# Performance work log

Measured on AMD Instinct MI355X. Metric: run time of the kernel, lower is better.

Reference implementation:

```python
import jax, jax.numpy as jnp
import numpy as np

B, C, H, W = 2, 64, 128, 128
HEADS, DH = 8, 32
DN = ('NCHW', 'OIHW', 'NCHW')


def _conv(x, w, pad):
    return jax.lax.conv_general_dilated(x, w, (1, 1), [(pad, pad), (pad, pad)], dimension_numbers=DN)


def _rconv3(x, w):
    # Conv3x3 module: ReflectionPad2d(1) then 3x3 VALID conv, no bias
    xp = jnp.pad(x, ((0, 0), (0, 0), (1, 1), (1, 1)), mode='reflect')
    return jax.lax.conv_general_dilated(xp, w, (1, 1), 'VALID', dimension_numbers=DN)


def _prelu(x, a):
    return jnp.where(x > 0, x, a * x)


def _l2n(x):
    # F.normalize(p=2, dim=-1), eps=1e-12
    return x / jnp.maximum(jnp.linalg.norm(x, axis=-1, keepdims=True), 1e-12)


def _ln(y, g, b):
    mu = y.mean(-1, keepdims=True)
    v = ((y - mu) ** 2).mean(-1, keepdims=True)
    return (y - mu) / jnp.sqrt(v + 1e-5) * g + b


def _qco(x, w1, sw, sb, t1w, t1b, t2w, t2b):
    # QCO_C with level_num == C
    b, Cc = x.shape[0], x.shape[1]
    L = Cc
    x1 = _rconv3(x, w1)
    x_ave = _conv(jnp.mean(x1, (2, 3), keepdims=True), sw, 0) + sb[None, :, None, None]  # [b,C,1,1]
    xq = x_ave.reshape(b, Cc)
    mn = xq.min(-1, keepdims=True)
    mx = xq.max(-1, keepdims=True)
    qs = jnp.arange(L, dtype=x.dtype)
    ql = (2.0 * qs + 1.0) / (2.0 * L) * (mx - mn) + mn  # [b,L]
    inter = (ql[:, 1] - ql[:, 0])[:, None, None]  # [b,1,1]
    quant = 1.0 - jnp.abs(ql[:, None, :] - xq[:, :, None])  # [b,C,L]
    quant = quant * (quant > 1.0 - inter)
    sta = quant.sum(1)  # [b,L]
    sta = sta / sta.sum(-1, keepdims=True)
    out = jnp.concatenate([sta[:, :, None, None], x_ave], axis=1)  # [b,2C,1,1]
    out = jax.nn.relu(_conv(out, t1w, 0) + t1b[None, :, None, None])
    out = jax.nn.relu(_conv(out, t2w, 0) + t2b[None, :, None, None])
    return out  # [b,C,1,1]


def _attention(x, w_down, w_mid, w_up, wq_l, wk_m, wv_m, wq_h, rescale,
               w_proj_l, b_proj_l, w_proj_h, b_proj_h,
               qco_w1, qco_sca_w, qco_sca_b, qco_t1_w, qco_t1_b, qco_t2_w, qco_t2_b,
               rsp_w1, rsp_prelu, rsp_w2, c31_w1, c31_prelu, c31_w2, c31_w3):
    b, Cc, Hh, Ww = x.shape
    n = Hh * Ww
    # QKV conv projections (Conv2d, zero pad 1, no bias)
    xCL = jnp.moveaxis(_conv(x, w_down, 1), 1, -1)  # [b,h,w,C]
    xCM = jnp.moveaxis(_conv(x, w_mid, 1), 1, -1)   # [b,h,w,2C]
    xCH = jnp.moveaxis(_conv(x, w_up, 1), 1, -1)    # [b,h,w,3C]
    xL = xCL.reshape(b, n, Cc)
    xM = xCM.reshape(b, n, 2 * Cc)
    xH = xCH.reshape(b, n, 3 * Cc)

    def to_heads(t, d):  # [b,n,heads*d] -> [b,heads,d,n]
        return t.reshape(b, n, HEADS, d).transpose(0, 2, 3, 1)

    q_l = _l2n(to_heads(xL @ wq_l.T, DH))            # [b,heads,DH,n]
    k_m = _l2n(to_heads(xM @ wk_m.T, 2 * DH))        # [b,heads,2DH,n]
    v_m = to_heads(xM @ wv_m.T, 2 * DH)              # [b,heads,2DH,n]
    q_h = _l2n(to_heads(xH @ wq_h.T, 3 * DH))        # [b,heads,3DH,n]

    attn_l = jax.nn.softmax(jnp.einsum('bhdn,bhen->bhde', q_l, k_m) * rescale, axis=-1)  # [b,heads,DH,2DH]
    attn_h = jax.nn.softmax(jnp.einsum('bhdn,bhen->bhde', q_h, k_m) * rescale, axis=-1)  # [b,heads,3DH,2DH]

    x_l = jnp.einsum('bhde,bhen->bhdn', attn_l, v_m).transpose(0, 3, 1, 2).reshape(b, n, HEADS * DH)
    x_h = jnp.einsum('bhde,bhen->bhdn', attn_h, v_m).transpose(0, 3, 1, 2).reshape(b, n, HEADS * 3 * DH)
    # NOTE: torch code does .view(b, c, h, w) on [b, n, c] output -> raw memory reinterpretation,
    # which is exactly jnp.reshape here (faithful to the original, including this quirk).
    out_cl = (x_l @ w_proj_l.T + b_proj_l).reshape(b, Cc, Hh, Ww)
    out_ch = (x_h @ w_proj_h.T + b_proj_h).reshape(b, 3 * Cc, Hh, Ww)

    Hcat = jnp.concatenate([out_cl, out_ch], axis=1)  # [b,4C,h,w]
    H_out = _rconv3(_prelu(_rconv3(Hcat, rsp_w1), rsp_prelu), rsp_w2)  # ReshapeBlock -> [b,C,h,w]
    att_before = _qco(jnp.moveaxis(xCL, -1, 1), qco_w1, qco_sca_w, qco_sca_b,
                      qco_t1_w, qco_t1_b, qco_t2_w, qco_t2_b)  # [b,C,1,1]
    t = _prelu(_rconv3(H_out, c31_w1), c31_prelu)
    H_add = _conv(_rconv3(t, c31_w2), c31_w3, 0)  # Conv3_1
    return H_add + H_out * att_before


def _ff_block(z, g, bb, w1, b1, w2, b2):
    # PreNorm(LayerNorm over channel) + FeedForward(Linear, LeakyReLU(0.01), Linear)
    y = jnp.moveaxis(z, 1, -1)
    y = _ln(y, g, bb)
    y = y @ w1.T + b1
    y = jnp.where(y > 0, y, 0.01 * y)
    y = y @ w2.T + b2
    return jnp.moveaxis(y, -1, 1)


def _forward(x, w_down, w_mid, w_up, wq_l, wk_m, wv_m, wq_h, rescale,
             w_proj_l, b_proj_l, w_proj_h, b_proj_h,
             qco_w1, qco_sca_w, qco_sca_b, qco_t1_w, qco_t1_b, qco_t2_w, qco_t2_b,
             rsp_w1, rsp_prelu, rsp_w2, c31_w1, c31_prelu, c31_w2, c31_w3,
             ln1_g, ln1_b, ff1_w1, ff1_b1, ff1_w2, ff1_b2,
             ln2_g, ln2_b, ff2_w1, ff2_b1, ff2_w2, ff2_b2):
    out1 = _attention(x, w_down, w_mid, w_up, wq_l, wk_m, wv_m, wq_h, rescale,
                      w_proj_l, b_proj_l, w_proj_h, b_proj_h,
                      qco_w1, qco_sca_w, qco_sca_b, qco_t1_w, qco_t1_b, qco_t2_w, qco_t2_b,
                      rsp_w1, rsp_prelu, rsp_w2, c31_w1, c31_prelu, c31_w2, c31_w3) + x
    out2 = _ff_block(out1, ln1_g, ln1_b, ff1_w1, ff1_b1, ff1_w2, ff1_b2) + out1
    out3 = _ff_block(out2, ln2_g, ln2_b, ff2_w1, ff2_b1, ff2_w2, ff2_b2) + out1
    return out3


def setup_inputs() -> dict:
    keys = iter(jax.random.split(jax.random.key(0), 48))

    def rn(shape, s=0.05):
        return (jax.random.normal(next(keys), shape, jnp.float32) * s)

    d = {
        'x': rn((B, C, H, W), 1.0),
        'w_down': rn((C, C, 3, 3)), 'w_mid': rn((2 * C, C, 3, 3)), 'w_up': rn((3 * C, C, 3, 3)),
        'wq_l': rn((HEADS * DH, C)), 'wk_m': rn((2 * HEADS * DH, 2 * C)),
        'wv_m': rn((2 * HEADS * DH, 2 * C)), 'wq_h': rn((3 * HEADS * DH, 3 * C)),
        'rescale': jnp.ones((HEADS, 1, 1), jnp.float32),
        'w_proj_l': rn((C, HEADS * DH)), 'b_proj_l': rn((C,)),
        'w_proj_h': rn((3 * C, 3 * HEADS * DH)), 'b_proj_h': rn((3 * C,)),
        'qco_w1': rn((C, C, 3, 3)), 'qco_sca_w': rn((C, C, 1, 1)), 'qco_sca_b': rn((C,)),
        'qco_t1_w': rn((C, 2 * C, 1, 1)), 'qco_t1_b': rn((C,)),
        'qco_t2_w': rn((C, C, 1, 1)), 'qco_t2_b': rn((C,)),
        'rsp_w1': rn((C, 4 * C, 3, 3)), 'rsp_prelu': jnp.array(0.25, jnp.float32), 'rsp_w2': rn((C, C, 3, 3)),
        'c31_w1': rn((C, C, 3, 3)), 'c31_prelu': jnp.array(0.25, jnp.float32),
        'c31_w2': rn((C, C, 3, 3)), 'c31_w3': rn((C, C, 1, 1)),
        'ln1_g': jnp.ones((C,), jnp.float32), 'ln1_b': jnp.zeros((C,), jnp.float32),
        'ff1_w1': rn((C, C)), 'ff1_b1': rn((C,)), 'ff1_w2': rn((C, C)), 'ff1_b2': rn((C,)),
        'ln2_g': jnp.ones((C,), jnp.float32), 'ln2_b': jnp.zeros((C,), jnp.float32),
        'ff2_w1': rn((C, C)), 'ff2_b1': rn((C,)), 'ff2_w2': rn((C, C)), 'ff2_b2': rn((C,)),
    }
    return d


def reference(x, w_down, w_mid, w_up, wq_l, wk_m, wv_m, wq_h, rescale,
              w_proj_l, b_proj_l, w_proj_h, b_proj_h,
              qco_w1, qco_sca_w, qco_sca_b, qco_t1_w, qco_t1_b, qco_t2_w, qco_t2_b,
              rsp_w1, rsp_prelu, rsp_w2, c31_w1, c31_prelu, c31_w2, c31_w3,
              ln1_g, ln1_b, ff1_w1, ff1_b1, ff1_w2, ff1_b2,
              ln2_g, ln2_b, ff2_w1, ff2_b1, ff2_w2, ff2_b2):
    return _forward(x, w_down, w_mid, w_up, wq_l, wk_m, wv_m, wq_h, rescale,
                    w_proj_l, b_proj_l, w_proj_h, b_proj_h,
                    qco_w1, qco_sca_w, qco_sca_b, qco_t1_w, qco_t1_b, qco_t2_w, qco_t2_b,
                    rsp_w1, rsp_prelu, rsp_w2, c31_w1, c31_prelu, c31_w2, c31_w3,
                    ln1_g, ln1_b, ff1_w1, ff1_b1, ff1_w2, ff1_b2,
                    ln2_g, ln2_b, ff2_w1, ff2_b1, ff2_w2, ff2_b2)
```

## Files before the change

kernel.cpp:

```cpp
#include <hip/hip_runtime.h>
#include <hip/hip_bf16.h>
#include <stdint.h>

typedef __hip_bfloat16 bf16;
typedef __attribute__((ext_vector_type(8))) __bf16 bf8v;
typedef __attribute__((ext_vector_type(8))) short short8;
typedef __attribute__((ext_vector_type(4))) short short4v;
typedef __attribute__((ext_vector_type(4))) float f32x4;
#define DEVINL __device__ __forceinline__
#define MFMA16(a,b,c) __builtin_amdgcn_mfma_f32_16x16x32_bf16((a),(b),(c),0,0,0)

DEVINL short f2bs(float f) { bf16 h = __float2bfloat16(f); return *reinterpret_cast<short*>(&h); }
DEVINL float bs2f(short s) { bf16 h = *reinterpret_cast<bf16*>(&s); return __bfloat162float(h); }


static const size_t OFF_ZBF   = 0;
static const size_t OFF_WTQ   = 29360128;
static const size_t OFF_WTR1  = 29802496;
static const size_t OFF_WTR2  = 30097408;
static const size_t OFF_WTC1  = 30171136;
static const size_t OFF_WTF   = 30244864;
static const size_t OFF_W1T   = 30318592;
static const size_t OFF_SCAWT = 30466048;
static const size_t OFF_T1WT  = 30482432;
static const size_t OFF_T2WT  = 30515200;
static const size_t OFF_GB    = 31645696;
static const size_t OFF_WQLB  = 32235520;
static const size_t OFF_WKMB  = 32268288;
static const size_t OFF_WQHB  = 32399360;
static const size_t OFF_T1    = 41082880;
static const size_t OFF_UL    = 41345024;
static const size_t OFF_UK    = 41476096;
static const size_t OFF_T1H   = 42000384;
static const size_t OFF_UH    = 42786816;
static const size_t OFF_WEL   = 44503040;
static const size_t OFF_WEH   = 44765184;
static const size_t OFF_ACATB = 45813760;
static const size_t OFF_TSUM  = 45944832;
static const size_t OFF_ATTB  = 45949440;
static const size_t OFF_HCATB = 45949952;
static const size_t OFF_MIDB  = 62727168;
static const size_t OFF_HOUTB = 66921472;
static const size_t OFF_WFFB  = 71115776;
static const size_t OFF_GPART = 79504384;
static const size_t OFF_HCATT = 79504384;
static const size_t OFF_XT    = 98378752;
static const size_t WS_BYTES  = 102573056;

__global__ __launch_bounds__(256) void k_prep_all(
    const float* __restrict__ wd, const float* __restrict__ wm,
    const float* __restrict__ wu, const float* __restrict__ rw1,
    const float* __restrict__ rw2, const float* __restrict__ cw1,
    const float* __restrict__ wql, const float* __restrict__ wkm,
    const float* __restrict__ wqh,
    const float* __restrict__ c31w3, const float* __restrict__ c31w2,
    const float* __restrict__ qw1, const float* __restrict__ qscaw,
    const float* __restrict__ qt1w, const float* __restrict__ qt2w,
    const float* __restrict__ f11, const float* __restrict__ f12,
    const float* __restrict__ f21, const float* __restrict__ f22,
    const float* __restrict__ x,
    bf16* __restrict__ wtq, bf16* __restrict__ wtr1,
    bf16* __restrict__ wtr2, bf16* __restrict__ wtc1,
    bf16* __restrict__ wqlb, bf16* __restrict__ wkmb,
    bf16* __restrict__ wqhb, bf16* __restrict__ wtf,
    float* __restrict__ w1t, float* __restrict__ scawt,
    float* __restrict__ t1wt, float* __restrict__ t2wt,
    bf16* __restrict__ wffb, short* __restrict__ xt) {
  __shared__ short sT[64][72];
  const int t = threadIdx.x;
  if (blockIdx.x >= 3040) {
    const int j = blockIdx.x - 3040;
    const int b = j >> 8, p0 = (j & 255) * 64;
    for (int i = t; i < 1024; i += 256) {
      int c = i >> 4, p4 = (i & 15) * 4;
      float4 g = *(const float4*)&x[(((size_t)(b * 64 + c)) << 14) + p0 + p4];
      sT[p4 + 0][c] = f2bs(g.x);
      sT[p4 + 1][c] = f2bs(g.y);
      sT[p4 + 2][c] = f2bs(g.z);
      sT[p4 + 3][c] = f2bs(g.w);
    }
    __syncthreads();
    for (int i = t; i < 512; i += 256) {
      int p = i >> 3, co = (i & 7) * 8;
      *(short8*)&xt[((((size_t)b << 14) + p0 + p)) * 64 + co] = *(short8*)&sT[p][co];
    }
    return;
  }
  int i = blockIdx.x * 256 + t;
  if (i < 221184) {
    int tap = i / 24576, r = i % 24576, oc = r >> 6, ic = r & 63;
    float v;
    if (oc < 64)       v = wd[(oc * 64 + ic) * 9 + tap];
    else if (oc < 192) v = wm[((oc - 64) * 64 + ic) * 9 + tap];
    else               v = wu[((oc - 192) * 64 + ic) * 9 + tap];
    wtq[i] = __float2bfloat16(v);
  } else if (i < 368640) {
    int j = i - 221184;
    int tap = j / 16384, r = j % 16384, oc = r >> 8, ic = r & 255;
    wtr1[j] = __float2bfloat16(rw1[(oc * 256 + ic) * 9 + tap]);
  } else if (i < 405504) {
    int j = i - 368640;
    int tap = j / 4096, r = j % 4096, oc = r >> 6, ic = r & 63;
    wtr2[j] = __float2bfloat16(rw2[(oc * 64 + ic) * 9 + tap]);
  } else if (i < 442368) {
    int j = i - 405504;
    int tap = j / 4096, r = j % 4096, oc = r >> 6, ic = r & 63;
    wtc1[j] = __float2bfloat16(cw1[(oc * 64 + ic) * 9 + tap]);
  } else if (i < 458752) {
    int j = i - 442368; wqlb[j] = __float2bfloat16(wql[j]);
  } else if (i < 524288) {
    int j = i - 458752; wkmb[j] = __float2bfloat16(wkm[j]);
  } else if (i < 671744) {
    int j = i - 524288; wqhb[j] = __float2bfloat16(wqh[j]);
  } else if (i < 708608) {
    int j = i - 671744;
    int tap = j / 4096, r = j % 4096, o = r >> 6, ic = r & 63;
    float s = 0.f;
    for (int m = 0; m < 64; m++)
      s = fmaf(c31w3[o * 64 + m], c31w2[(m * 64 + ic) * 9 + tap], s);
    wtf[j] = __float2bfloat16(s);
  } else if (i < 745472) {
    int o = i - 708608;
    int c = o & 63, rest = o >> 6, jj = rest / 9, tap = rest % 9;
    w1t[o] = qw1[(c * 64 + jj) * 9 + tap];
  } else if (i < 749568) {
    int o = i - 745472;
    int c = o & 63, jj = o >> 6;
    scawt[o] = qscaw[c * 64 + jj];
  } else if (i < 757760) {
    int o = i - 749568;
    int c = o & 63, jj = o >> 6;
    t1wt[o] = qt1w[c * 128 + jj];
  } else if (i < 761856) {
    int o = i - 757760;
    int c = o & 63, jj = o >> 6;
    t2wt[o] = qt2w[c * 64 + jj];
  } else if (i < 778240) {
    int j = i - 761856;
    int stage = j >> 12, r = j & 4095;
    const float* src = (stage == 0) ? f11 : (stage == 1) ? f12 : (stage == 2) ? f21 : f22;
    wffb[j] = __float2bfloat16(src[r]);
  }
}

__global__ __launch_bounds__(256) void k_transph(const short* __restrict__ hc,
                                                 short* __restrict__ ht) {
  __shared__ short sT[64][72];
  const int t = threadIdx.x, b = blockIdx.z, p0 = blockIdx.x * 64, c0 = blockIdx.y * 64;
  for (int i = t; i < 512; i += 256) {
    int c = i >> 3, qo = (i & 7) * 8;
    short8 v = *(const short8*)&hc[(((size_t)(b * 256 + c0 + c)) << 14) + p0 + qo];
#pragma unroll
    for (int u = 0; u < 8; u++) sT[qo + u][c] = v[u];
  }
  __syncthreads();
  for (int i = t; i < 512; i += 256) {
    int q = i >> 3, co = (i & 7) * 8;
    *(short8*)&ht[((size_t)(b * 16384 + p0 + q)) * 256 + c0 + co] = *(short8*)&sT[q][co];
  }
}

__global__ __launch_bounds__(256) void k_convq(
    const short* __restrict__ xt, const short* __restrict__ wtq,
    bf16* __restrict__ zbf)
{
  __shared__ short sX[3][130][72];
  const int t = threadIdx.x, lane = t & 63, wv = t >> 6;
  const int y = blockIdx.x, ocg = blockIdx.y, b = blockIdx.z;

  for (int i = t; i < 3120; i += 256) {
    int ko = i & 7, c2 = i >> 3, col = c2 % 130, row = c2 / 130;
    int gy = y + row - 1, gx = col - 1;
    short8 vv;
    if ((gy >= 0) & (gy < 128) & (gx >= 0) & (gx < 128)) {
      vv = *(const short8*)&xt[((size_t)b * 1048576 + (size_t)((gy << 7) + gx) * 64) + ko * 8];
    } else {
#pragma unroll
      for (int u = 0; u < 8; u++) vv[u] = 0;
    }
    *(short8*)&sX[row][col][ko * 8] = vv;
  }
  __syncthreads();

  const f32x4 zero = {0.f, 0.f, 0.f, 0.f};
  f32x4 acc[3][8];
#pragma unroll
  for (int m = 0; m < 3; m++)
#pragma unroll
    for (int n = 0; n < 8; n++) acc[m][n] = zero;

#pragma unroll
  for (int tap = 0; tap < 9; tap++) {
    const int ky = tap / 3, kx = tap % 3;
#pragma unroll
    for (int kk = 0; kk < 2; kk++) {
      const int kb = kk * 32 + (lane >> 4) * 8;
      bf8v a0 = *(const bf8v*)&wtq[(size_t)((tap * 384 + ocg * 192 + wv * 48 + (lane & 15)) * 64) + kb];
      bf8v a1 = *(const bf8v*)&wtq[(size_t)((tap * 384 + ocg * 192 + wv * 48 + 16 + (lane & 15)) * 64) + kb];
      bf8v a2 = *(const bf8v*)&wtq[(size_t)((tap * 384 + ocg * 192 + wv * 48 + 32 + (lane & 15)) * 64) + kb];
#pragma unroll
      for (int n = 0; n < 8; n++) {
        bf8v bfr = *(const bf8v*)&sX[ky][n * 16 + (lane & 15) + kx][kb];
        acc[0][n] = MFMA16(a0, bfr, acc[0][n]);
        acc[1][n] = MFMA16(a1, bfr, acc[1][n]);
        acc[2][n] = MFMA16(a2, bfr, acc[2][n]);
      }
    }
  }
  __syncthreads();
  short* sO = &sX[0][0][0];
#pragma unroll
  for (int m = 0; m < 3; m++) {
    const int ocl = wv * 48 + m * 16 + ((lane >> 4) << 2);
#pragma unroll
    for (int n = 0; n < 8; n++) {
      const int px = n * 16 + (lane & 15);
      sO[(ocl + 0) * 132 + px] = f2bs(acc[m][n][0]);
      sO[(ocl + 1) * 132 + px] = f2bs(acc[m][n][1]);
      sO[(ocl + 2) * 132 + px] = f2bs(acc[m][n][2]);
      sO[(ocl + 3) * 132 + px] = f2bs(acc[m][n][3]);
    }
  }
  __syncthreads();
  for (int i = t; i < 3072; i += 256) {
    int ocl = i >> 4, px8 = (i & 15) * 8;
    *(short8*)&zbf[(((size_t)(b * 384 + ocg * 192 + ocl)) << 14) + (y << 7) + px8] =
        *(short8*)&sO[ocl * 132 + px8];
  }
}

template<int EPI>
__global__ __launch_bounds__(256) void k_conv64(
    const short* __restrict__ in, int str, long bstride, int Cin,
    const short* __restrict__ Wt,
    short* __restrict__ outb,
    const float* __restrict__ prelu_a)
{
  __shared__ short sX[3][66][72];
  const int t = threadIdx.x, lane = t & 63, wv = t >> 6;
  const int y = blockIdx.x, x0 = blockIdx.y * 64, b = blockIdx.z;

  const f32x4 zero = {0.f, 0.f, 0.f, 0.f};
  f32x4 acc[4] = {zero, zero, zero, zero};

  for (int icb = 0; icb < Cin; icb += 64) {
    __syncthreads();
    for (int i = t; i < 1584; i += 256) {
      int ko = i & 7, c2 = i >> 3, col = c2 % 66, row = c2 / 66;
      int gy = y + row - 1, gx = x0 + col - 1;
      gy = gy < 0 ? 1 : (gy > 127 ? 126 : gy);
      gx = gx < 0 ? 1 : (gx > 127 ? 126 : gx);
      *(short8*)&sX[row][col][ko * 8] =
          *(const short8*)&in[(size_t)b * bstride + (size_t)((gy << 7) + gx) * str + icb + ko * 8];
    }
    __syncthreads();
#pragma unroll
    for (int tap = 0; tap < 9; tap++) {
      const int ky = tap / 3, kx = tap % 3;
#pragma unroll
      for (int kk = 0; kk < 2; kk++) {
        const int kb = kk * 32 + (lane >> 4) * 8;
        bf8v afr = *(const bf8v*)&Wt[(size_t)(tap * 64 + wv * 16 + (lane & 15)) * Cin + icb + kb];
#pragma unroll
        for (int n = 0; n < 4; n++) {
          bf8v bfr = *(const bf8v*)&sX[ky][n * 16 + (lane & 15) + kx][kb];
          acc[n] = MFMA16(afr, bfr, acc[n]);
        }
      }
    }
  }
  const int oc0 = wv * 16 + ((lane >> 4) << 2);
  const float aP = (EPI == 1) ? prelu_a[0] : 0.f;
#pragma unroll
  for (int n = 0; n < 4; n++) {
    const int gpx = (y << 7) + x0 + n * 16 + (lane & 15);
    short4v ss;
#pragma unroll
    for (int r = 0; r < 4; r++) {
      float v = acc[n][r];
      if (EPI == 1) v = v > 0.f ? v : aP * v;
      ss[r] = f2bs(v);
    }
    *(short4v*)&outb[((size_t)(b * 16384 + gpx)) * 64 + oc0] = ss;
  }
}

__global__ __launch_bounds__(256) void k_convff(
    const short* __restrict__ in,
    const short* __restrict__ Wt,
    const short* __restrict__ houtpm,
    const float* __restrict__ attb,
    const float* __restrict__ x_nchw,
    const short* __restrict__ wffb,
    const float* __restrict__ g1, const float* __restrict__ be1,
    const float* __restrict__ b11, const float* __restrict__ b12,
    const float* __restrict__ g2, const float* __restrict__ be2,
    const float* __restrict__ b21, const float* __restrict__ b22,
    float* __restrict__ outp)
{
  __shared__ short sX[3][66][72];
  __shared__ float sv[64][68];
  __shared__ short sy[64][72];
  __shared__ float spar[8][64];
  const int t = threadIdx.x, lane = t & 63, wv = t >> 6;
  const int y = blockIdx.x, x0 = blockIdx.y * 64, b = blockIdx.z;

  if (t < 64) {
    spar[0][t] = g1[t]; spar[1][t] = be1[t]; spar[2][t] = b11[t]; spar[3][t] = b12[t];
    spar[4][t] = g2[t]; spar[5][t] = be2[t]; spar[6][t] = b21[t]; spar[7][t] = b22[t];
  }
  for (int i = t; i < 1584; i += 256) {
    int ko = i & 7, c2 = i >> 3, col = c2 % 66, row = c2 / 66;
    int gy = y + row - 1, gx = x0 + col - 1;
    gy = gy < 0 ? 1 : (gy > 127 ? 126 : gy);
    gx = gx < 0 ? 1 : (gx > 127 ? 126 : gx);
    *(short8*)&sX[row][col][ko * 8] =
        *(const short8*)&in[(size_t)b * 1048576 + (size_t)((gy << 7) + gx) * 64 + ko * 8];
  }
  __syncthreads();

  const f32x4 zero = {0.f, 0.f, 0.f, 0.f};
  {
    f32x4 cacc[4] = {zero, zero, zero, zero};
#pragma unroll
    for (int tap = 0; tap < 9; tap++) {
      const int ky = tap / 3, kx = tap % 3;
#pragma unroll
      for (int kk = 0; kk < 2; kk++) {
        const int kb = kk * 32 + (lane >> 4) * 8;
        bf8v afr = *(const bf8v*)&Wt[(size_t)(tap * 64 + wv * 16 + (lane & 15)) * 64 + kb];
#pragma unroll
        for (int n = 0; n < 4; n++) {
          bf8v bfr = *(const bf8v*)&sX[ky][n * 16 + (lane & 15) + kx][kb];
          cacc[n] = MFMA16(afr, bfr, cacc[n]);
        }
      }
    }
    const int oc0 = wv * 16 + ((lane >> 4) << 2);
    float4 av = *(const float4*)&attb[b * 64 + oc0];
#pragma unroll
    for (int n = 0; n < 4; n++) {
      const int pxl = n * 16 + (lane & 15);
      const int gpx = (y << 7) + x0 + pxl;
      short4v hv = *(const short4v*)&houtpm[((size_t)(b * 16384 + gpx)) * 64 + oc0];
#pragma unroll
      for (int r = 0; r < 4; r++)
        sv[pxl][oc0 + r] = cacc[n][r] + bs2f(hv[r]) * (&av.x)[r] +
                           x_nchw[(((size_t)(b * 64 + oc0 + r)) << 14) + gpx];
    }
  }
  __syncthreads();

  const int chq = ((lane >> 4) << 2);
  const int pxl = wv * 16 + (lane & 15);
  float4 vv[4];
#pragma unroll
  for (int m = 0; m < 4; m++) vv[m] = *(const float4*)&sv[pxl][m * 16 + chq];

  f32x4 facc[4];

#define LN_F(SRCV, GI, BI)                                                      \
  {                                                                             \
    float s1 = 0.f, s2 = 0.f;                                                   \
    _Pragma("unroll")                                                           \
    for (int m = 0; m < 4; m++)                                                 \
      _Pragma("unroll")                                                         \
      for (int r = 0; r < 4; r++) {                                             \
        float vx = (&SRCV[m].x)[r];                                             \
        s1 += vx; s2 += vx * vx;                                                \
      }                                                                         \
    s1 += __shfl_xor(s1, 16); s1 += __shfl_xor(s1, 32);                         \
    s2 += __shfl_xor(s2, 16); s2 += __shfl_xor(s2, 32);                         \
    float mu = s1 * (1.f / 64.f);                                               \
    float var = fmaxf(s2 * (1.f / 64.f) - mu * mu, 0.f);                        \
    float rstd = 1.f / sqrtf(var + 1e-5f);                                      \
    _Pragma("unroll")                                                           \
    for (int m = 0; m < 4; m++) {                                               \
      short4v ss;                                                               \
      _Pragma("unroll")                                                         \
      for (int r = 0; r < 4; r++) {                                             \
        int ch = m * 16 + chq + r;                                              \
        ss[r] = f2bs(((&SRCV[m].x)[r] - mu) * rstd * spar[GI][ch] + spar[BI][ch]); \
      }                                                                         \
      *(short4v*)&sy[pxl][m * 16 + chq] = ss;                                   \
    }                                                                           \
  }

#define MM_F(SIDX)                                                              \
  {                                                                             \
    _Pragma("unroll")                                                           \
    for (int m = 0; m < 4; m++) facc[m] = zero;                                 \
    _Pragma("unroll")                                                           \
    for (int kk = 0; kk < 2; kk++) {                                            \
      const int kb = kk * 32 + (lane >> 4) * 8;                                 \
      bf8v bfr = *(const bf8v*)&sy[wv * 16 + (lane & 15)][kb];                  \
      _Pragma("unroll")                                                         \
      for (int m = 0; m < 4; m++) {                                             \
        bf8v afr = *(const bf8v*)&wffb[(size_t)(SIDX) * 4096 +                  \
                                       (m * 16 + (lane & 15)) * 64 + kb];       \
        facc[m] = MFMA16(afr, bfr, facc[m]);                                    \
      }                                                                         \
    }                                                                           \
  }

  LN_F(vv, 0, 1);
  MM_F(0);
#pragma unroll
  for (int m = 0; m < 4; m++) {
    short4v ss;
#pragma unroll
    for (int r = 0; r < 4; r++) {
      float h = facc[m][r] + spar[2][m * 16 + chq + r];
      h = h > 0.f ? h : 0.01f * h;
      ss[r] = f2bs(h);
    }
    *(short4v*)&sy[pxl][m * 16 + chq] = ss;
  }
  MM_F(1);
  float4 o2v[4];
#pragma unroll
  for (int m = 0; m < 4; m++)
#pragma unroll
    for (int r = 0; r < 4; r++)
      (&o2v[m].x)[r] = facc[m][r] + spar[3][m * 16 + chq + r] + (&vv[m].x)[r];
  LN_F(o2v, 4, 5);
  MM_F(2);
#pragma unroll
  for (int m = 0; m < 4; m++) {
    short4v ss;
#pragma unroll
    for (int r = 0; r < 4; r++) {
      float h = facc[m][r] + spar[6][m * 16 + chq + r];
      h = h > 0.f ? h : 0.01f * h;
      ss[r] = f2bs(h);
    }
    *(short4v*)&sy[pxl][m * 16 + chq] = ss;
  }
  MM_F(3);
  const int gpx = (y << 7) + x0 + pxl;
#pragma unroll
  for (int m = 0; m < 4; m++)
#pragma unroll
    for (int r = 0; r < 4; r++) {
      const int ch = m * 16 + chq + r;
      outp[(((size_t)(b * 64 + ch)) << 14) + gpx] =
          facc[m][r] + spar[7][ch] + (&vv[m].x)[r];
    }
#undef LN_F
#undef MM_F
}

__global__ __launch_bounds__(256) void k_gramm(const short* __restrict__ Z,
                                               float* __restrict__ Gp) {
  static const char TIa[18] = {0,0,0,1,1,2,1,1,1,2,2,2,3,3,3,4,4,5};
  static const char TJa[18] = {0,1,2,1,2,2,3,4,5,3,4,5,3,4,5,4,5,5};
  const int ti = TIa[blockIdx.x], tj = TJa[blockIdx.x];
  const int kc = blockIdx.y, b = blockIdx.z;
  __shared__ short sA[64][72];
  __shared__ short sB[64][72];
  const int t = threadIdx.x, lane = t & 63, wv = t >> 6;
  const int wo = wv & 1, wp = wv >> 1;
  const f32x4 zero = {0.f, 0.f, 0.f, 0.f};
  f32x4 acc[2][2];
#pragma unroll
  for (int m = 0; m < 2; m++)
#pragma unroll
    for (int n = 0; n < 2; n++) acc[m][n] = zero;
  const size_t zb = (size_t)b * 6291456;
  const int k0 = kc * 1024;
  for (int ks = 0; ks < 1024; ks += 64) {
    __syncthreads();
    for (int i = t; i < 512; i += 256) {
      int r = i >> 3, ko = i & 7;
      *(short8*)&sA[r][ko * 8] =
          *(const short8*)&Z[zb + ((size_t)(ti * 64 + r) << 14) + k0 + ks + ko * 8];
      *(short8*)&sB[r][ko * 8] =
          *(const short8*)&Z[zb + ((size_t)(tj * 64 + r) << 14) + k0 + ks + ko * 8];
    }
    __syncthreads();
#pragma unroll
    for (int kk = 0; kk < 2; kk++) {
      const int kb = kk * 32 + (lane >> 4) * 8;
      bf8v bfr[2];
#pragma unroll
      for (int n = 0; n < 2; n++)
        bfr[n] = *(const bf8v*)&sB[wp * 32 + n * 16 + (lane & 15)][kb];
#pragma unroll
      for (int m = 0; m < 2; m++) {
        bf8v afr = *(const bf8v*)&sA[wo * 32 + m * 16 + (lane & 15)][kb];
#pragma unroll
        for (int n = 0; n < 2; n++)
          acc[m][n] = MFMA16(afr, bfr[n], acc[m][n]);
      }
    }
  }
  float* gp = Gp + ((size_t)(kc * 2 + b)) * 147456;
#pragma unroll
  for (int m = 0; m < 2; m++)
#pragma unroll
    for (int n = 0; n < 2; n++)
#pragma unroll
      for (int r = 0; r < 4; r++) {
        const int row = ti * 64 + wo * 32 + m * 16 + ((lane >> 4) << 2) + r;
        const int col = tj * 64 + wp * 32 + n * 16 + (lane & 15);
        float v = acc[m][n][r];
        gp[(size_t)row * 384 + col] = v;
        if (ti != tj) gp[(size_t)col * 384 + row] = v;
      }
}

__global__ __launch_bounds__(256) void k_gt(const float* __restrict__ Gp,
                                            bf16* __restrict__ Gb,
                                            const bf16* __restrict__ Z,
                                            float* __restrict__ Tsum) {
  __shared__ float sc[16];
  __shared__ float red[4][9];
  const int t = threadIdx.x;
  if (blockIdx.x < 1152) {
    int i = blockIdx.x * 256 + t;
    if (i >= 294912) return;
    int b = i / 147456, e = i % 147456;
    float s = 0.f;
#pragma unroll
    for (int c = 0; c < 16; c++) s += Gp[(size_t)(c * 2 + b) * 147456 + e];
    Gb[(size_t)b * 147456 + e] = __float2bfloat16(s);
    return;
  }
  const int bid = blockIdx.x - 1152;
  const int c = bid & 63, b = bid >> 6;
  const bf16* src = Z + (((size_t)(b * 384 + c)) << 14);
  float a9[9] = {};
  for (int i = t; i < 2048; i += 256) {
    int y = i >> 4, x0 = (i & 15) * 8;
    short8 v8 = *(const short8*)&src[(y << 7) + x0];
    float vs[8], s8 = 0.f;
#pragma unroll
    for (int u = 0; u < 8; u++) { vs[u] = bs2f(v8[u]); s8 += vs[u]; }
    a9[0] += s8;
    int ri = (y == 0) ? 0 : (y == 1) ? 1 : (y == 126) ? 2 : (y == 127) ? 3 : -1;
    if (ri >= 0) a9[1 + ri] += s8;
    if (x0 == 0)   { a9[5] += vs[0]; a9[6] += vs[1]; }
    if (x0 == 120) { a9[7] += vs[6]; a9[8] += vs[7]; }
    if (ri >= 0) {
      if (x0 == 0)   { sc[ri * 4 + 0] = vs[0]; sc[ri * 4 + 1] = vs[1]; }
      if (x0 == 120) { sc[ri * 4 + 2] = vs[6]; sc[ri * 4 + 3] = vs[7]; }
    }
  }
#pragma unroll
  for (int q = 0; q < 9; q++)
#pragma unroll
    for (int o = 32; o; o >>= 1) a9[q] += __shfl_xor(a9[q], o);
  const int w = t >> 6;
  if ((t & 63) == 0)
#pragma unroll
    for (int q = 0; q < 9; q++) red[w][q] = a9[q];
  __syncthreads();
  if (t == 0) {
    float s9[9];
#pragma unroll
    for (int q = 0; q < 9; q++) s9[q] = red[0][q] + red[1][q] + red[2][q] + red[3][q];
    const float T = s9[0];
    float R[4] = {s9[1], s9[2], s9[3], s9[4]};
    const float C0 = s9[5], C1 = s9[6], C126 = s9[7], C127 = s9[8];
    float rs[4][3];
#pragma unroll
    for (int ri = 0; ri < 4; ri++) {
      rs[ri][0] = R[ri] - sc[ri * 4 + 3] + sc[ri * 4 + 1];
      rs[ri][1] = R[ri];
      rs[ri][2] = R[ri] - sc[ri * 4 + 0] + sc[ri * 4 + 2];
    }
    float A3[3] = {T - C127 + C1, T, T - C0 + C126};
#pragma unroll
    for (int dx = 0; dx < 3; dx++) {
      Tsum[bid * 9 + 0 * 3 + dx] = A3[dx] - rs[3][dx] + rs[1][dx];
      Tsum[bid * 9 + 1 * 3 + dx] = A3[dx];
      Tsum[bid * 9 + 2 * 3 + dx] = A3[dx] - rs[0][dx] + rs[2][dx];
    }
  }
}

struct MJobs5 {
  const short* A[5];
  float* C[5];
  int lda[5], K[5], r0[5], c0[5], ldc[5];
  long sC[5];
  int nx[5], b0[6];
};

__global__ __launch_bounds__(256) void k_mgemm5(MJobs5 J, const short* __restrict__ Gb) {
  const int bx = blockIdx.x, z = blockIdx.y;
  int j = 0;
  while (bx >= J.b0[j + 1]) j++;
  const int local = bx - J.b0[j];
  const int xn = local % J.nx[j], ym = local / J.nx[j];
  const int t = threadIdx.x, lane = t & 63, wv = t >> 6;
  const short* Gp = Gb + (size_t)z * 147456;
  const short* Ap = J.A[j];
  const int K = J.K[j], lda = J.lda[j];
  const int m0 = ym * 64 + wv * 16, n0 = xn * 64;
  const int gc0 = J.c0[j] + n0, r0 = J.r0[j];
  const f32x4 zero = {0.f, 0.f, 0.f, 0.f};
  f32x4 acc[4] = {zero, zero, zero, zero};
  for (int kk = 0; kk < K; kk += 32) {
    const int kb = kk + (lane >> 4) * 8;
    bf8v afr = *(const bf8v*)&Ap[(size_t)(m0 + (lane & 15)) * lda + kb];
#pragma unroll
    for (int n = 0; n < 4; n++) {
      bf8v bfr = *(const bf8v*)&Gp[(size_t)(gc0 + n * 16 + (lane & 15)) * 384 + r0 + kb];
      acc[n] = MFMA16(afr, bfr, acc[n]);
    }
  }
  float* Cp = J.C[j] + (size_t)z * J.sC[j];
  const int mq = m0 + ((lane >> 4) << 2);
#pragma unroll
  for (int n = 0; n < 4; n++) {
    const int nc = n0 + n * 16 + (lane & 15);
#pragma unroll
    for (int r = 0; r < 4; r++)
      Cp[(size_t)(mq + r) * J.ldc[j] + nc] = acc[n][r];
  }
}

__global__ __launch_bounds__(256) void k_pixm(
    const short* __restrict__ Z, const short* __restrict__ Acatb,
    const float* __restrict__ bl, const float* __restrict__ bh,
    bf16* __restrict__ hcat)
{
  const int p0 = blockIdx.x * 64, ocg = blockIdx.y, b = blockIdx.z;
  __shared__ short sA[64][136];
  __shared__ short sB[64][136];
  const int t = threadIdx.x, lane = t & 63, wv = t >> 6;
  for (int i = t; i < 1024; i += 256) {
    int oc = i >> 4, ko = i & 15;
    *(short8*)&sA[oc][ko * 8] =
        *(const short8*)&Acatb[((size_t)(b * 256 + ocg * 64 + oc)) * 128 + ko * 8];
  }
  for (int i = t; i < 1024; i += 256) {
    int px = i & 63, ko = i >> 6;
    short8 vv;
#pragma unroll
    for (int u = 0; u < 8; u++)
      vv[u] = Z[((size_t)(b * 384 + 64 + ko * 8 + u) << 14) + p0 + px];
    *(short8*)&sB[px][ko * 8] = vv;
  }
  __syncthreads();
  const f32x4 zero = {0.f, 0.f, 0.f, 0.f};
  f32x4 acc[4] = {zero, zero, zero, zero};
#pragma unroll
  for (int kk = 0; kk < 4; kk++) {
    const int kb = kk * 32 + (lane >> 4) * 8;
    bf8v afr = *(const bf8v*)&sA[wv * 16 + (lane & 15)][kb];
#pragma unroll
    for (int n = 0; n < 4; n++) {
      bf8v bfr = *(const bf8v*)&sB[n * 16 + (lane & 15)][kb];
      acc[n] = MFMA16(afr, bfr, acc[n]);
    }
  }
  const size_t hbase = (size_t)b * 4194304;
#pragma unroll
  for (int n = 0; n < 4; n++) {
    const int px = p0 + n * 16 + (lane & 15);
#pragma unroll
    for (int r = 0; r < 4; r++) {
      const int oc = ocg * 64 + wv * 16 + ((lane >> 4) << 2) + r;
      float v = acc[n][r] + (oc < 64 ? bl[oc] : bh[oc - 64]);
      size_t addr = (oc < 64) ? hbase + (size_t)px * 64 + oc
                              : hbase + 1048576 + (size_t)px * 192 + (oc - 64);
      hcat[addr] = __float2bfloat16(v);
    }
  }
}

struct Jobs2 {
  const float* A[2]; const float* B[2];
  int K[2]; int lda[2];
  long sB[2];
  int nx[2]; int b0[3]; int co[2];
};

__global__ __launch_bounds__(256) void k_sgemm2b(Jobs2 J, bf16* __restrict__ Cb) {
  __shared__ float sa[16][17];
  __shared__ float sb[16][17];
  const int bx = blockIdx.x, z = blockIdx.y;
  int j = (bx >= J.b0[1]) ? 1 : 0;
  const int local = bx - J.b0[j];
  const int x = local % J.nx[j], y = local / J.nx[j];
  const int tx = threadIdx.x & 15, ty = threadIdx.x >> 4;
  const float* Ap = J.A[j];
  const float* Bp = J.B[j] + (size_t)z * J.sB[j];
  const int K = J.K[j], lda = J.lda[j];
  const int m = y * 16 + ty, n = x * 16 + tx;
  float acc = 0.f;
  for (int k0 = 0; k0 < K; k0 += 16) {
    sa[ty][tx] = Ap[(size_t)m * lda + k0 + tx];
    sb[ty][tx] = Bp[(size_t)(k0 + ty) * 128 + n];
    __syncthreads();
#pragma unroll
    for (int kk = 0; kk < 16; kk++) acc = fmaf(sa[ty][kk], sb[kk][tx], acc);
    __syncthreads();
  }
  Cb[(size_t)z * 32768 + J.co[j] + (size_t)m * 128 + n] = __float2bfloat16(acc);
}

__global__ __launch_bounds__(512) void k_attnw(
    const float* __restrict__ T1, const float* __restrict__ T1H,
    const float* __restrict__ UL, const float* __restrict__ UK,
    const float* __restrict__ UH,
    const float* __restrict__ wql, const float* __restrict__ wkm,
    const float* __restrict__ wqh, const float* __restrict__ wvm,
    const float* __restrict__ rescale,
    float* __restrict__ WeL, float* __restrict__ WeH,
    const float* __restrict__ Tsum, const float* __restrict__ w1t,
    const float* __restrict__ scawt, const float* __restrict__ scab,
    const float* __restrict__ t1wt, const float* __restrict__ t1b,
    const float* __restrict__ t2wt, const float* __restrict__ t2b,
    float* __restrict__ attb)
{
  __shared__ float sK[64 * 132];
  __shared__ float sQ[32 * 132];
  __shared__ float sAt[32 * 64];
  __shared__ float sNk[64];
  __shared__ float sNq[32];
  __shared__ float sm[64], sxq[64], scat[128], sh1[64];
  const int t = threadIdx.x, b = blockIdx.y;

  if (blockIdx.x == 32) {
    const int c = t;
    if (t < 64) {
      float acc = 0.f;
      for (int j = 0; j < 64; j++) {
#pragma unroll
        for (int tap = 0; tap < 9; tap++)
          acc = fmaf(w1t[((j * 9 + tap) << 6) + c], Tsum[(b * 64 + j) * 9 + tap], acc);
      }
      sm[c] = acc * (1.f / 16384.f);
    }
    __syncthreads();
    if (t < 64) {
      float xa = scab[c];
      for (int j = 0; j < 64; j++) xa = fmaf(scawt[(j << 6) + c], sm[j], xa);
      sxq[c] = xa;
    }
    __syncthreads();
    if (t < 64) {
      float xa = sxq[c];
      float mn = xa, mx = xa;
#pragma unroll
      for (int o = 32; o; o >>= 1) {
        mn = fminf(mn, __shfl_xor(mn, o));
        mx = fmaxf(mx, __shfl_xor(mx, o));
      }
      float inter = (mx - mn) * (1.f / 64.f);
      float ql = (2.f * c + 1.f) / 128.f * (mx - mn) + mn;
      float sta = 0.f;
      for (int j = 0; j < 64; j++) {
        float q = 1.f - fabsf(ql - sxq[j]);
        sta += (q > 1.f - inter) ? q : 0.f;
      }
      float tot = sta;
#pragma unroll
      for (int o = 32; o; o >>= 1) tot += __shfl_xor(tot, o);
      sta = sta / fmaxf(tot, 1e-30f);
      scat[c] = sta; scat[64 + c] = xa;
    }
    __syncthreads();
    if (t < 64) {
      float h = t1b[c];
      for (int j = 0; j < 128; j++) h = fmaf(t1wt[(j << 6) + c], scat[j], h);
      h = fmaxf(h, 0.f);
      sh1[c] = h;
    }
    __syncthreads();
    if (t < 64) {
      float o2 = t2b[c];
      for (int j = 0; j < 64; j++) o2 = fmaf(t2wt[(j << 6) + c], sh1[j], o2);
      attb[b * 64 + c] = fmaxf(o2, 0.f);
    }
    return;
  }

  const int h = blockIdx.x >> 2, cy = blockIdx.x & 3;
  const int isL = (cy == 0);
  const int rbase = isL ? 0 : (cy - 1) * 32;
  const float* TQ = isL ? (T1 + (size_t)(b * 256 + h * 32) * 128)
                        : (T1H + (size_t)(b * 768 + h * 96 + rbase) * 128);
  for (int idx = t; idx < 8192; idx += 512) {
    int e = idx >> 7, k = idx & 127;
    sK[e * 132 + k] = wkm[(size_t)(h * 64 + e) * 128 + k];
  }
  for (int idx = t; idx < 4096; idx += 512) {
    int r = idx >> 7, k = idx & 127;
    sQ[r * 132 + k] = TQ[(size_t)r * 128 + k];
  }
  __syncthreads();

  if (t < 64) {
    const float4* u4 = (const float4*)(UK + (size_t)(b * 512 + h * 64 + t) * 128);
    const float4* k4 = (const float4*)&sK[t * 132];
    float s = 0.f;
    for (int q = 0; q < 32; q++) {
      float4 a = u4[q], c = k4[q];
      s = fmaf(a.x, c.x, s); s = fmaf(a.y, c.y, s);
      s = fmaf(a.z, c.z, s); s = fmaf(a.w, c.w, s);
    }
    sNk[t] = fmaxf(sqrtf(fmaxf(s, 0.f)), 1e-12f);
  } else if (t >= 128 && t < 160) {
    const int r = t - 128;
    const float* u; const float* wv; int K;
    if (isL) { K = 64;  u = UL + (size_t)(b * 256 + h * 32 + r) * 64;
               wv = wql + (size_t)(h * 32 + r) * 64; }
    else     { K = 192; u = UH + (size_t)(b * 768 + h * 96 + rbase + r) * 192;
               wv = wqh + (size_t)(h * 96 + rbase + r) * 192; }
    const float4* u4 = (const float4*)u;
    const float4* w4 = (const float4*)wv;
    float s = 0.f;
    for (int q = 0; q < (K >> 2); q++) {
      float4 a = u4[q], c = w4[q];
      s = fmaf(a.x, c.x, s); s = fmaf(a.y, c.y, s);
      s = fmaf(a.z, c.z, s); s = fmaf(a.w, c.w, s);
    }
    sNq[r] = fmaxf(sqrtf(fmaxf(s, 0.f)), 1e-12f);
  }
  __syncthreads();

  const int w = t >> 6, lane = t & 63;
  const float rs = rescale[h];
  for (int r = w; r < 32; r += 8) {
    const float4* q4 = (const float4*)&sQ[r * 132];
    const float4* k4 = (const float4*)&sK[lane * 132];
    float s = 0.f;
#pragma unroll
    for (int q = 0; q < 32; q++) {
      float4 a = q4[q], c = k4[q];
      s = fmaf(a.x, c.x, s); s = fmaf(a.y, c.y, s);
      s = fmaf(a.z, c.z, s); s = fmaf(a.w, c.w, s);
    }
    float logit = s / (sNq[r] * sNk[lane]) * rs;
    float m = logit;
#pragma unroll
    for (int o = 32; o; o >>= 1) m = fmaxf(m, __shfl_xor(m, o));
    float p = __expf(logit - m);
    float den = p;
#pragma unroll
    for (int o = 32; o; o >>= 1) den += __shfl_xor(den, o);
    sAt[r * 64 + lane] = p / den;
  }
  __syncthreads();

  const int jg = t & 31, rw = t >> 5;
  const float* Vh = wvm + (size_t)(h * 64) * 128;
  float* dst = isL ? (WeL + (size_t)(b * 256 + h * 32) * 128)
                   : (WeH + (size_t)(b * 768 + h * 96 + rbase) * 128);
  for (int r = rw; r < 32; r += 16) {
    float4 acc = make_float4(0.f, 0.f, 0.f, 0.f);
    for (int e = 0; e < 64; e++) {
      float a = sAt[r * 64 + e];
      float4 v4 = *(const float4*)&Vh[(size_t)e * 128 + jg * 4];
      acc.x = fmaf(a, v4.x, acc.x);
      acc.y = fmaf(a, v4.y, acc.y);
      acc.z = fmaf(a, v4.z, acc.z);
      acc.w = fmaf(a, v4.w, acc.w);
    }
    *(float4*)&dst[(size_t)r * 128 + jg * 4] = acc;
  }
}

extern "C" void kernel_launch(void* const* d_in, const int* in_sizes, int n_in,
                              void* d_out, int out_size, void* d_ws, size_t ws_size,
                              hipStream_t stream)
{
  if (ws_size < WS_BYTES) return;
  char* ws = (char*)d_ws;

  const float* x       = (const float*)d_in[0];
  const float* w_down  = (const float*)d_in[1];
  const float* w_mid   = (const float*)d_in[2];
  const float* w_up    = (const float*)d_in[3];
  const float* wq_l    = (const float*)d_in[4];
  const float* wk_m    = (const float*)d_in[5];
  const float* wv_m    = (const float*)d_in[6];
  const float* wq_h    = (const float*)d_in[7];
  const float* rescale = (const float*)d_in[8];
  const float* w_proj_l= (const float*)d_in[9];
  const float* b_proj_l= (const float*)d_in[10];
  const float* w_proj_h= (const float*)d_in[11];
  const float* b_proj_h= (const float*)d_in[12];
  const float* qco_w1  = (const float*)d_in[13];
  const float* qsca_w  = (const float*)d_in[14];
  const float* qsca_b  = (const float*)d_in[15];
  const float* qt1_w   = (const float*)d_in[16];
  const float* qt1_b   = (const float*)d_in[17];
  const float* qt2_w   = (const float*)d_in[18];
  const float* qt2_b   = (const float*)d_in[19];
  const float* rsp_w1  = (const float*)d_in[20];
  const float* rsp_pr  = (const float*)d_in[21];
  const float* rsp_w2  = (const float*)d_in[22];
  const float* c31_w1  = (const float*)d_in[23];
  const float* c31_pr  = (const float*)d_in[24];
  const float* c31_w2  = (const float*)d_in[25];
  const float* c31_w3  = (const float*)d_in[26];
  const float* ln1_g   = (const float*)d_in[27];
  const float* ln1_b   = (const float*)d_in[28];
  const float* ff1_w1  = (const float*)d_in[29];
  const float* ff1_b1  = (const float*)d_in[30];
  const float* ff1_w2  = (const float*)d_in[31];
  const float* ff1_b2  = (const float*)d_in[32];
  const float* ln2_g   = (const float*)d_in[33];
  const float* ln2_b   = (const float*)d_in[34];
  const float* ff2_w1  = (const float*)d_in[35];
  const float* ff2_b1  = (const float*)d_in[36];
  const float* ff2_w2  = (const float*)d_in[37];
  const float* ff2_b2  = (const float*)d_in[38];

  bf16*  zbf   = (bf16*)(ws + OFF_ZBF);
  bf16*  wtq   = (bf16*)(ws + OFF_WTQ);
  bf16*  wtr1  = (bf16*)(ws + OFF_WTR1);
  bf16*  wtr2  = (bf16*)(ws + OFF_WTR2);
  bf16*  wtc1  = (bf16*)(ws + OFF_WTC1);
  bf16*  wtf   = (bf16*)(ws + OFF_WTF);
  float* w1t   = (float*)(ws + OFF_W1T);
  float* scawt = (float*)(ws + OFF_SCAWT);
  float* t1wt  = (float*)(ws + OFF_T1WT);
  float* t2wt  = (float*)(ws + OFF_T2WT);
  bf16*  Gb    = (bf16*)(ws + OFF_GB);
  bf16*  wqlb  = (bf16*)(ws + OFF_WQLB);
  bf16*  wkmb  = (bf16*)(ws + OFF_WKMB);
  bf16*  wqhb  = (bf16*)(ws + OFF_WQHB);
  float* gpart = (float*)(ws + OFF_GPART);
  float* T1    = (float*)(ws + OFF_T1);
  float* UL    = (float*)(ws + OFF_UL);
  float* UK    = (float*)(ws + OFF_UK);
  float* T1H   = (float*)(ws + OFF_T1H);
  float* UH    = (float*)(ws + OFF_UH);
  float* WeL   = (float*)(ws + OFF_WEL);
  float* WeH   = (float*)(ws + OFF_WEH);
  bf16*  acatb = (bf16*)(ws + OFF_ACATB);
  float* tsum  = (float*)(ws + OFF_TSUM);
  float* attb  = (float*)(ws + OFF_ATTB);
  bf16*  hcatb = (bf16*)(ws + OFF_HCATB);
  short* hcatT = (short*)(ws + OFF_HCATT);
  short* midb  = (short*)(ws + OFF_MIDB);
  short* houtb = (short*)(ws + OFF_HOUTB);
  bf16*  wffb  = (bf16*)(ws + OFF_WFFB);
  short* xt    = (short*)(ws + OFF_XT);

  k_prep_all<<<dim3(3552), 256, 0, stream>>>(
      w_down, w_mid, w_up, rsp_w1, rsp_w2, c31_w1, wq_l, wk_m, wq_h,
      c31_w3, c31_w2, qco_w1, qsca_w, qt1_w, qt2_w,
      ff1_w1, ff1_w2, ff2_w1, ff2_w2, x,
      wtq, wtr1, wtr2, wtc1, wqlb, wkmb, wqhb, wtf,
      w1t, scawt, t1wt, t2wt, wffb, xt);

  k_convq<<<dim3(128, 2, 2), 256, 0, stream>>>(xt, (const short*)wtq, zbf);

  k_gramm<<<dim3(18, 16, 2), 256, 0, stream>>>((const short*)zbf, gpart);

  k_gt<<<dim3(1280), 256, 0, stream>>>(gpart, Gb, zbf, tsum);

  MJobs5 M5;
  M5.A[0] = (const short*)wqlb; M5.lda[0] = 64;  M5.K[0] = 64;  M5.r0[0] = 0;   M5.c0[0] = 64;  M5.C[0] = T1;  M5.ldc[0] = 128; M5.sC[0] = 32768;  M5.nx[0] = 2;
  M5.A[1] = (const short*)wqlb; M5.lda[1] = 64;  M5.K[1] = 64;  M5.r0[1] = 0;   M5.c0[1] = 0;   M5.C[1] = UL;  M5.ldc[1] = 64;  M5.sC[1] = 16384;  M5.nx[1] = 1;
  M5.A[2] = (const short*)wkmb; M5.lda[2] = 128; M5.K[2] = 128; M5.r0[2] = 64;  M5.c0[2] = 64;  M5.C[2] = UK;  M5.ldc[2] = 128; M5.sC[2] = 65536;  M5.nx[2] = 2;
  M5.A[3] = (const short*)wqhb; M5.lda[3] = 192; M5.K[3] = 192; M5.r0[3] = 192; M5.c0[3] = 64;  M5.C[3] = T1H; M5.ldc[3] = 128; M5.sC[3] = 98304;  M5.nx[3] = 2;
  M5.A[4] = (const short*)wqhb; M5.lda[4] = 192; M5.K[4] = 192; M5.r0[4] = 192; M5.c0[4] = 192; M5.C[4] = UH;  M5.ldc[4] = 192; M5.sC[4] = 147456; M5.nx[4] = 3;
  M5.b0[0] = 0; M5.b0[1] = 8; M5.b0[2] = 12; M5.b0[3] = 28; M5.b0[4] = 52; M5.b0[5] = 88;
  k_mgemm5<<<dim3(88, 2), 256, 0, stream>>>(M5, (const short*)Gb);

  k_attnw<<<dim3(33, 2), 512, 0, stream>>>(
      T1, T1H, UL, UK, UH, wq_l, wk_m, wq_h, wv_m, rescale, WeL, WeH,
      tsum, w1t, scawt, qsca_b, t1wt, qt1_b, t2wt, qt2_b, attb);

  Jobs2 J2;
  J2.A[0] = w_proj_l; J2.B[0] = WeL; J2.K[0] = 256; J2.lda[0] = 256; J2.sB[0] = 32768; J2.nx[0] = 8; J2.co[0] = 0;
  J2.A[1] = w_proj_h; J2.B[1] = WeH; J2.K[1] = 768; J2.lda[1] = 768; J2.sB[1] = 98304; J2.nx[1] = 8; J2.co[1] = 8192;
  J2.b0[0] = 0; J2.b0[1] = 32; J2.b0[2] = 128;
  k_sgemm2b<<<dim3(128, 2), 256, 0, stream>>>(J2, acatb);

  k_pixm<<<dim3(256, 4, 2), 256, 0, stream>>>((const short*)zbf, (const short*)acatb,
                                              b_proj_l, b_proj_h, hcatb);

  k_transph<<<dim3(256, 4, 2), 256, 0, stream>>>((const short*)hcatb, hcatT);

  k_conv64<1><<<dim3(128, 2, 2), 256, 0, stream>>>(
      hcatT, 256, 4194304L, 256, (const short*)wtr1, midb, rsp_pr);
  k_conv64<0><<<dim3(128, 2, 2), 256, 0, stream>>>(
      midb, 64, 1048576L, 64, (const short*)wtr2, houtb, nullptr);

  k_conv64<1><<<dim3(128, 2, 2), 256, 0, stream>>>(
      houtb, 64, 1048576L, 64, (const short*)wtc1, midb, c31_pr);

  k_convff<<<dim3(128, 2, 2), 256, 0, stream>>>(
      midb, (const short*)wtf, houtb, attb, x, (const short*)wffb,
      ln1_g, ln1_b, ff1_b1, ff1_b2, ln2_g, ln2_b, ff2_b1, ff2_b2,
      (float*)d_out);
}
```

Baseline: 231.5 us.

## Remap gram blocks per XCD, share diagonal tiles, and batch attention dot rows

```diff
diff --git a/kernel.cpp b/kernel.cpp
--- a/kernel.cpp
+++ b/kernel.cpp
@@ -454,10 +454,18 @@
                                                float* __restrict__ Gp) {
   static const char TIa[18] = {0,0,0,1,1,2,1,1,1,2,2,2,3,3,3,4,4,5};
   static const char TJa[18] = {0,1,2,1,2,2,3,4,5,3,4,5,3,4,5,4,5,5};
-  const int ti = TIa[blockIdx.x], tj = TJa[blockIdx.x];
-  const int kc = blockIdx.y, b = blockIdx.z;
+  const int L = blockIdx.x;
+  const int xcd = L & 7;
+  const int rest = L >> 3;
+  const int p = rest % 18;
+  const int ghi = rest / 18;
+  const int g = xcd + 8 * ghi;
+  const int kc = g & 15, b = g >> 4;
+  const int ti = TIa[p], tj = TJa[p];
+  const bool diag = (ti == tj);
   __shared__ short sA[64][72];
   __shared__ short sB[64][72];
+  short (*sBp)[72] = diag ? sA : sB;
   const int t = threadIdx.x, lane = t & 63, wv = t >> 6;
   const int wo = wv & 1, wp = wv >> 1;
   const f32x4 zero = {0.f, 0.f, 0.f, 0.f};
@@ -474,8 +482,9 @@
       int r = i >> 3, ko = i & 7;
       *(short8*)&sA[r][ko * 8] =
           *(const short8*)&Z[zb + ((size_t)(ti * 64 + r) << 14) + k0 + ks + ko * 8];
-      *(short8*)&sB[r][ko * 8] =
-          *(const short8*)&Z[zb + ((size_t)(tj * 64 + r) << 14) + k0 + ks + ko * 8];
+      if (!diag)
+        *(short8*)&sB[r][ko * 8] =
+            *(const short8*)&Z[zb + ((size_t)(tj * 64 + r) << 14) + k0 + ks + ko * 8];
     }
     __syncthreads();
 #pragma unroll
@@ -484,7 +493,7 @@
       bf8v bfr[2];
 #pragma unroll
       for (int n = 0; n < 2; n++)
-        bfr[n] = *(const bf8v*)&sB[wp * 32 + n * 16 + (lane & 15)][kb];
+        bfr[n] = *(const bf8v*)&sBp[wp * 32 + n * 16 + (lane & 15)][kb];
 #pragma unroll
       for (int m = 0; m < 2; m++) {
         bf8v afr = *(const bf8v*)&sA[wo * 32 + m * 16 + (lane & 15)][kb];
@@ -825,25 +834,40 @@
 
   const int w = t >> 6, lane = t & 63;
   const float rs = rescale[h];
-  for (int r = w; r < 32; r += 8) {
-    const float4* q4 = (const float4*)&sQ[r * 132];
+  {
     const float4* k4 = (const float4*)&sK[lane * 132];
-    float s = 0.f;
+    const float4* q40 = (const float4*)&sQ[(w)      * 132];
+    const float4* q41 = (const float4*)&sQ[(w + 8)  * 132];
+    const float4* q42 = (const float4*)&sQ[(w + 16) * 132];
+    const float4* q43 = (const float4*)&sQ[(w + 24) * 132];
+    float s0 = 0.f, s1 = 0.f, s2 = 0.f, s3 = 0.f;
 #pragma unroll
     for (int q = 0; q < 32; q++) {
-      float4 a = q4[q], c = k4[q];
-      s = fmaf(a.x, c.x, s); s = fmaf(a.y, c.y, s);
-      s = fmaf(a.z, c.z, s); s = fmaf(a.w, c.w, s);
-    }
-    float logit = s / (sNq[r] * sNk[lane]) * rs;
-    float m = logit;
-#pragma unroll
-    for (int o = 32; o; o >>= 1) m = fmaxf(m, __shfl_xor(m, o));
-    float p = __expf(logit - m);
-    float den = p;
-#pragma unroll
-    for (int o = 32; o; o >>= 1) den += __shfl_xor(den, o);
-    sAt[r * 64 + lane] = p / den;
+      float4 c = k4[q];
+      float4 a;
+      a = q40[q]; s0 = fmaf(a.x, c.x, s0); s0 = fmaf(a.y, c.y, s0);
+                  s0 = fmaf(a.z, c.z, s0); s0 = fmaf(a.w, c.w, s0);
+      a = q41[q]; s1 = fmaf(a.x, c.x, s1); s1 = fmaf(a.y, c.y, s1);
+                  s1 = fmaf(a.z, c.z, s1); s1 = fmaf(a.w, c.w, s1);
+      a = q42[q]; s2 = fmaf(a.x, c.x, s2); s2 = fmaf(a.y, c.y, s2);
+                  s2 = fmaf(a.z, c.z, s2); s2 = fmaf(a.w, c.w, s2);
+      a = q43[q]; s3 = fmaf(a.x, c.x, s3); s3 = fmaf(a.y, c.y, s3);
+                  s3 = fmaf(a.z, c.z, s3); s3 = fmaf(a.w, c.w, s3);
+    }
+    float ss[4] = {s0, s1, s2, s3};
+#pragma unroll
+    for (int j = 0; j < 4; j++) {
+      const int r = w + j * 8;
+      float logit = ss[j] / (sNq[r] * sNk[lane]) * rs;
+      float m = logit;
+#pragma unroll
+      for (int o = 32; o; o >>= 1) m = fmaxf(m, __shfl_xor(m, o));
+      float p = __expf(logit - m);
+      float den = p;
+#pragma unroll
+      for (int o = 32; o; o >>= 1) den += __shfl_xor(den, o);
+      sAt[r * 64 + lane] = p / den;
+    }
   }
   __syncthreads();
 
@@ -953,7 +977,7 @@
 
   k_convq<<<dim3(128, 2, 2), 256, 0, stream>>>(xt, (const short*)wtq, zbf);
 
-  k_gramm<<<dim3(18, 16, 2), 256, 0, stream>>>((const short*)zbf, gpart);
+  k_gramm<<<dim3(576), 256, 0, stream>>>((const short*)zbf, gpart);
 
   k_gt<<<dim3(1280), 256, 0, stream>>>(gpart, Gb, zbf, tsum);
 
```

New measurement: 228.7 us (median of 3 runs). About the same (-1.2%).
